# Performance work log

Measured on AMD Instinct MI355X. Metric: run time of the kernel, lower is better.

Reference implementation:

```python
import jax, jax.numpy as jnp
import numpy as np

N_NODES = 50000
N_EDGES = 800000
IN_DIM = 256
OUT_DIM = 64
HEADS = 4
NEG_SLOPE = 0.2  # PyG GATConv default


def setup_inputs() -> dict:
    key = jax.random.key(0)
    k_x, k_e, k_w, k_as, k_ad = jax.random.split(key, 5)
    x = jax.random.normal(k_x, (N_NODES, IN_DIM), dtype=jnp.float32)
    edge_index = jax.random.randint(k_e, (2, N_EDGES), 0, N_NODES, dtype=jnp.int64)
    # Glorot-ish scaled params (as in PyG GATConv)
    W = jax.random.normal(k_w, (IN_DIM, HEADS * OUT_DIM), dtype=jnp.float32) / np.sqrt(IN_DIM)
    att_src = jax.random.normal(k_as, (HEADS, OUT_DIM), dtype=jnp.float32) / np.sqrt(OUT_DIM)
    att_dst = jax.random.normal(k_ad, (HEADS, OUT_DIM), dtype=jnp.float32) / np.sqrt(OUT_DIM)
    bias = jnp.zeros((HEADS * OUT_DIM,), dtype=jnp.float32)
    return {"x": x, "edge_index": edge_index, "W": W,
            "att_src": att_src, "att_dst": att_dst, "bias": bias}


def reference(x, edge_index, W, att_src, att_dst, bias):
    N = x.shape[0]
    H, C = att_src.shape
    # add self-loops (PyG GATConv default add_self_loops=True)
    loop = jnp.arange(N, dtype=edge_index.dtype)
    src = jnp.concatenate([edge_index[0], loop])  # [E+N] message sources j
    dst = jnp.concatenate([edge_index[1], loop])  # [E+N] message targets i

    xh = (x @ W).reshape(N, H, C)                 # [N, H, C]
    a_src = jnp.einsum('nhc,hc->nh', xh, att_src)  # [N, H]
    a_dst = jnp.einsum('nhc,hc->nh', xh, att_dst)  # [N, H]

    logits = jax.nn.leaky_relu(a_src[src] + a_dst[dst], NEG_SLOPE)  # [E+N, H]
    # segment softmax over incoming edges of each destination node
    seg_max = jax.ops.segment_max(logits, dst, num_segments=N)      # [N, H]
    e = jnp.exp(logits - seg_max[dst])
    seg_sum = jax.ops.segment_sum(e, dst, num_segments=N)           # [N, H]
    alpha = e / seg_sum[dst]                                        # [E+N, H]

    # weighted scatter-aggregate of source features
    msgs = alpha[:, :, None] * xh[src]                              # [E+N, H, C]
    out = jax.ops.segment_sum(msgs, dst, num_segments=N)            # [N, H, C]
    out = out.reshape(N, H * C) + bias                              # concat heads + bias
    # h.dim() == 2 here, so the original's mean(dim=1) branch is not taken
    return out
```

## Files before the change

### kernel.cpp

```cpp
#include <hip/hip_runtime.h>

#define NEG_SLOPE 0.2f
#define LRELU(x) ((x) > 0.0f ? (x) : NEG_SLOPE * (x))

typedef short short8 __attribute__((ext_vector_type(8)));
typedef unsigned short ushort8 __attribute__((ext_vector_type(8)));
typedef float f32x4v __attribute__((ext_vector_type(4)));

__device__ __forceinline__ unsigned short f2bf(float f) {
  unsigned int u = __float_as_uint(f);
  unsigned int r = (u + 0x7FFFu + ((u >> 16) & 1u)) >> 16;
  return (unsigned short)r;
}

__device__ __forceinline__ float bf2f(unsigned short u) {
  return __uint_as_float(((unsigned int)u) << 16);
}

__device__ __forceinline__ unsigned int cvt_pk_bf16(float lo, float hi) {
  unsigned int r;
  asm("v_cvt_pk_bf16_f32 %0, %1, %2" : "=v"(r) : "v"(lo), "v"(hi));
  return r;
}

__device__ __forceinline__ void gload_lds16(const void* g, void* l) {
  __builtin_amdgcn_global_load_lds(
      (const __attribute__((address_space(1))) unsigned int*)g,
      (__attribute__((address_space(3))) unsigned int*)l, 16, 0, 0);
}

#define CBC 448
#define CBW 64
#define CBF 512

__global__ __launch_bounds__(256) void fused_pre(
    const float* __restrict__ W, unsigned short* __restrict__ Wtb,
    const int* __restrict__ ei, int* __restrict__ deg, int E) {
  int b = blockIdx.x;
  int tid = threadIdx.x;
  if (b < CBC) {
    for (int e = b * 256 + tid; e < E; e += CBC * 256)
      atomicAdd(&deg[ei[E + e]], 1);
  } else {
    int bb = b - CBC;
    for (int idx = bb * 256 + tid; idx < 256 * 256; idx += CBW * 256) {
      int n = idx >> 8, k = idx & 255;
      Wtb[n * 256 + k] = f2bf(W[k * 256 + n]);
    }
  }
}

__global__ __launch_bounds__(1024) void scan1_kernel(const int* __restrict__ deg,
                                                     int* __restrict__ row_start,
                                                     int* __restrict__ bsum, int N) {
  __shared__ int buf[1024];
  int i = blockIdx.x * 1024 + (int)threadIdx.x;
  int v = (i < N) ? deg[i] : 0;
  buf[threadIdx.x] = v;
  __syncthreads();
  int run = v;
  for (int off = 1; off < 1024; off <<= 1) {
    int t = ((int)threadIdx.x >= off) ? buf[threadIdx.x - off] : 0;
    __syncthreads();
    run += t;
    buf[threadIdx.x] = run;
    __syncthreads();
  }
  if (i < N) row_start[i] = run - v;
  if (threadIdx.x == 1023) bsum[blockIdx.x] = run;
}

__global__ __launch_bounds__(1024) void scan_off(int* __restrict__ row_start,
                                                 const int* __restrict__ bsum,
                                                 int nb, int N) {
  __shared__ int s_off;
  int b = blockIdx.x;
  if (threadIdx.x < 64) {
    int acc = 0;
    for (int j = (int)threadIdx.x; j < b; j += 64) acc += bsum[j];
    for (int off = 32; off; off >>= 1) acc += __shfl_down(acc, off, 64);
    if (threadIdx.x == 0) s_off = acc;
  }
  __syncthreads();
  int off = s_off;
  int i = b * 1024 + (int)threadIdx.x;
  if (i < N) row_start[i] += off;
  if (b == nb - 1 && threadIdx.x == 0) row_start[N] = off + bsum[b];
}

__global__ __launch_bounds__(256) void fused_main(
    const float* __restrict__ Xf, const unsigned short* __restrict__ Wtb,
    const float* __restrict__ attS, const float* __restrict__ attD,
    unsigned short* __restrict__ XHb, float* __restrict__ a_src,
    float* __restrict__ a_dst,
    const int* __restrict__ ei, const int* __restrict__ row_start,
    int* __restrict__ cursor, int* __restrict__ csr_src,
    int nGemm, int E, int N) {
  __shared__ unsigned short lA[128 * 32];
  __shared__ unsigned short lB[128 * 32];
  const int bid = blockIdx.x;
  const int tid = threadIdx.x;

  if (bid >= nGemm) {
    int bb = bid - nGemm;
    for (int e = bb * 256 + tid; e < E; e += CBF * 256) {
      int d = ei[E + e];
      int slot = row_start[d] + atomicAdd(&cursor[d], 1);
      csr_src[slot] = ei[e];
    }
    return;
  }

  const int lane = tid & 63;
  const int wave = tid >> 6;
  const int n0 = (bid & 1) * 128;
  const int m0 = (bid >> 1) * 128;
  const int wr = (wave >> 1) * 64;
  const int wc = (wave & 1) * 64;

  f32x4v acc[4][4];
#pragma unroll
  for (int i = 0; i < 4; ++i)
#pragma unroll
    for (int j = 0; j < 4; ++j) acc[i][j] = (f32x4v)(0.0f);

  const int srow = tid >> 2;
  const int skb = (tid & 3) * 16;
  const float* ap0 = Xf + (size_t)min(m0 + (tid >> 2), N - 1) * 256 + (tid & 3) * 8;
  const float* ap1 = Xf + (size_t)min(m0 + 64 + (tid >> 2), N - 1) * 256 + (tid & 3) * 8;

  const char* WtC = (const char*)Wtb;
  char* lAc = (char*)&lA[0];
  char* lBc = (char*)&lB[0];
  const int ldsB0 = wave * 1024;
  const int lr = lane & 15;
  const int hq = lane >> 4;
  const int kq = hq * 16;

  float4 c0 = *reinterpret_cast<const float4*>(ap0);
  float4 c1 = *reinterpret_cast<const float4*>(ap0 + 4);
  float4 c2 = *reinterpret_cast<const float4*>(ap1);
  float4 c3 = *reinterpret_cast<const float4*>(ap1 + 4);

#pragma unroll
  for (int kk = 0; kk < 8; ++kk) {
    const int k0 = kk * 32;
    gload_lds16(WtC + (size_t)(n0 + srow) * 512 + (size_t)k0 * 2 + skb, lBc + ldsB0);
    gload_lds16(WtC + (size_t)(n0 + srow + 64) * 512 + (size_t)k0 * 2 + skb,
                lBc + ldsB0 + 4096);
    {
      uint4 w0, w1;
      w0.x = cvt_pk_bf16(c0.x, c0.y); w0.y = cvt_pk_bf16(c0.z, c0.w);
      w0.z = cvt_pk_bf16(c1.x, c1.y); w0.w = cvt_pk_bf16(c1.z, c1.w);
      w1.x = cvt_pk_bf16(c2.x, c2.y); w1.y = cvt_pk_bf16(c2.z, c2.w);
      w1.z = cvt_pk_bf16(c3.x, c3.y); w1.w = cvt_pk_bf16(c3.z, c3.w);
      *reinterpret_cast<uint4*>(lAc + tid * 16) = w0;
      *reinterpret_cast<uint4*>(lAc + 4096 + tid * 16) = w1;
    }
    if (kk < 7) {
      c0 = *reinterpret_cast<const float4*>(ap0 + k0 + 32);
      c1 = *reinterpret_cast<const float4*>(ap0 + k0 + 36);
      c2 = *reinterpret_cast<const float4*>(ap1 + k0 + 32);
      c3 = *reinterpret_cast<const float4*>(ap1 + k0 + 36);
    }
    __syncthreads();

    short8 a[4], b[4];
#pragma unroll
    for (int i = 0; i < 4; ++i)
      a[i] = *reinterpret_cast<const short8*>(lAc + (wr + i * 16 + lr) * 64 + kq);
#pragma unroll
    for (int j = 0; j < 4; ++j)
      b[j] = *reinterpret_cast<const short8*>(lBc + (wc + j * 16 + lr) * 64 + kq);
#pragma unroll
    for (int i = 0; i < 4; ++i)
#pragma unroll
      for (int j = 0; j < 4; ++j)
        acc[i][j] = __builtin_amdgcn_mfma_f32_16x16x32_bf16(a[i], b[j], acc[i][j], 0, 0, 0);
    __syncthreads();
  }

  const int h = (n0 + wc) >> 6;
  float ws_[4], wd_[4];
#pragma unroll
  for (int j = 0; j < 4; ++j) {
    ws_[j] = attS[h * 64 + j * 16 + lr];
    wd_[j] = attD[h * 64 + j * 16 + lr];
  }
  const int rbase = m0 + wr + hq * 4;

#pragma unroll
  for (int i = 0; i < 4; ++i) {
#pragma unroll
    for (int r = 0; r < 4; ++r) {
      float ps = 0.f, pd = 0.f;
#pragma unroll
      for (int j = 0; j < 4; ++j) {
        ps += acc[i][j][r] * ws_[j];
        pd += acc[i][j][r] * wd_[j];
      }
#pragma unroll
      for (int off = 1; off < 16; off <<= 1) {
        ps += __shfl_xor(ps, off, 64);
        pd += __shfl_xor(pd, off, 64);
      }
      int row = rbase + i * 16 + r;
      if (lr == 0 && row < N) {
        a_src[row * 4 + h] = ps;
        a_dst[row * 4 + h] = pd;
      }
    }
  }

#pragma unroll
  for (int i = 0; i < 4; ++i)
#pragma unroll
    for (int j = 0; j < 4; ++j) {
      int col = n0 + wc + j * 16 + lr;
#pragma unroll
      for (int r = 0; r < 4; ++r)
        XHb[(size_t)(rbase + i * 16 + r) * 256 + col] = f2bf(acc[i][j][r]);
    }
}

__global__ __launch_bounds__(256) void gat_agg(
    const unsigned short* __restrict__ XHb, const float* __restrict__ a_src,
    const float* __restrict__ a_dst, const int* __restrict__ row_start,
    const int* __restrict__ csr_src, const float* __restrict__ bias,
    float* __restrict__ out, int N) {
  int wid = threadIdx.x >> 6;
  int lane = threadIdx.x & 63;
  int node = blockIdx.x * 4 + wid;
  if (node >= N) return;

  const int half = lane >> 5;
  const int l5 = lane & 31;
  const int h = l5 >> 3;
  const int c = l5 << 3;
  const unsigned short* __restrict__ xrow = XHb + c;

  float ad_h = a_dst[node * 4 + h];
  float as_h = a_src[node * 4 + h];

  int start = row_start[node];
  int end = row_start[node + 1];

  float acc[8];
  float sw = 0.f;
  if (half == 0) {
    float wself = __expf(LRELU(as_h + ad_h));
    ushort8 sv = *reinterpret_cast<const ushort8*>(xrow + (size_t)node * 256);
#pragma unroll
    for (int k = 0; k < 8; ++k) acc[k] = wself * bf2f(sv[k]);
    sw = wself;
  } else {
#pragma unroll
    for (int k = 0; k < 8; ++k) acc[k] = 0.f;
  }

  int p = start;
  for (; p + 8 <= end; p += 8) {
    int s0 = csr_src[p + half];
    int s1 = csr_src[p + 2 + half];
    int s2 = csr_src[p + 4 + half];
    int s3 = csr_src[p + 6 + half];
    float a0 = a_src[s0 * 4 + h] + ad_h;
    float a1 = a_src[s1 * 4 + h] + ad_h;
    float a2 = a_src[s2 * 4 + h] + ad_h;
    float a3 = a_src[s3 * 4 + h] + ad_h;
    ushort8 u0 = *reinterpret_cast<const ushort8*>(xrow + (size_t)s0 * 256);
    ushort8 u1 = *reinterpret_cast<const ushort8*>(xrow + (size_t)s1 * 256);
    ushort8 u2 = *reinterpret_cast<const ushort8*>(xrow + (size_t)s2 * 256);
    ushort8 u3 = *reinterpret_cast<const ushort8*>(xrow + (size_t)s3 * 256);
    float w0 = __expf(LRELU(a0));
    float w1 = __expf(LRELU(a1));
    float w2 = __expf(LRELU(a2));
    float w3 = __expf(LRELU(a3));
#pragma unroll
    for (int k = 0; k < 8; ++k) {
      acc[k] += w0 * bf2f(u0[k]);
      acc[k] += w1 * bf2f(u1[k]);
      acc[k] += w2 * bf2f(u2[k]);
      acc[k] += w3 * bf2f(u3[k]);
    }
    sw += (w0 + w1) + (w2 + w3);
  }
#pragma unroll
  for (int k = 0; k < 4; ++k) {
    int idx = p + 2 * k + half;
    if (idx < end) {
      int s = csr_src[idx];
      float aa = a_src[s * 4 + h] + ad_h;
      ushort8 u = *reinterpret_cast<const ushort8*>(xrow + (size_t)s * 256);
      float ww = __expf(LRELU(aa));
#pragma unroll
      for (int q = 0; q < 8; ++q) acc[q] += ww * bf2f(u[q]);
      sw += ww;
    }
  }

  sw += __shfl_xor(sw, 32, 64);
#pragma unroll
  for (int k = 0; k < 8; ++k) acc[k] += __shfl_xor(acc[k], 32, 64);

  if (half == 0) {
    float inv = 1.0f / sw;
    float4 b0 = *reinterpret_cast<const float4*>(bias + c);
    float4 b1 = *reinterpret_cast<const float4*>(bias + c + 4);
    float4 o0, o1;
    o0.x = acc[0] * inv + b0.x; o0.y = acc[1] * inv + b0.y;
    o0.z = acc[2] * inv + b0.z; o0.w = acc[3] * inv + b0.w;
    o1.x = acc[4] * inv + b1.x; o1.y = acc[5] * inv + b1.y;
    o1.z = acc[6] * inv + b1.z; o1.w = acc[7] * inv + b1.w;
    *reinterpret_cast<float4*>(out + (size_t)node * 256 + c) = o0;
    *reinterpret_cast<float4*>(out + (size_t)node * 256 + c + 4) = o1;
  }
}

extern "C" void kernel_launch(void* const* d_in, const int* in_sizes, int n_in,
                              void* d_out, int out_size, void* d_ws, size_t ws_size,
                              hipStream_t stream) {
  const float* x    = (const float*)d_in[0];
  const int*   ei   = (const int*)d_in[1];
  const float* Wm   = (const float*)d_in[2];
  const float* attS = (const float*)d_in[3];
  const float* attD = (const float*)d_in[4];
  const float* bias = (const float*)d_in[5];
  float* out = (float*)d_out;

  const int N = in_sizes[0] / 256;
  const int E = in_sizes[1] / 2;
  const int Mp = (N + 127) / 128 * 128;
  const int nb = (N + 1023) / 1024;

  char* w = (char*)d_ws;
  unsigned short* XHb = (unsigned short*)w;  w += (size_t)Mp * 256 * 2;
  unsigned short* Wtb = (unsigned short*)w;  w += (size_t)256 * 256 * 2;
  float* a_src = (float*)w;                  w += (size_t)N * 4 * 4;
  float* a_dst = (float*)w;                  w += (size_t)N * 4 * 4;
  int* deg = (int*)w;                        w += (size_t)N * 4;
  int* cursor = (int*)w;                     w += (size_t)N * 4;
  int* row_start = (int*)w;                  w += ((size_t)(N + 1) * 4 + 255) / 256 * 256;
  int* bsum = (int*)w;                       w += ((size_t)nb * 4 + 255) / 256 * 256;
  int* csr_src = (int*)w;                    w += (size_t)E * 4;

  hipMemsetAsync(deg, 0, (size_t)2 * N * 4, stream);

  fused_pre<<<CBC + CBW, 256, 0, stream>>>(Wm, Wtb, ei, deg, E);

  scan1_kernel<<<nb, 1024, 0, stream>>>(deg, row_start, bsum, N);
  scan_off<<<nb, 1024, 0, stream>>>(row_start, bsum, nb, N);

  const int nGemm = 2 * (Mp / 128);
  fused_main<<<nGemm + CBF, 256, 0, stream>>>(x, Wtb, attS, attD, XHb, a_src, a_dst,
                                              ei, row_start, cursor, csr_src,
                                              nGemm, E, N);

  gat_agg<<<(N + 3) / 4, 256, 0, stream>>>(XHb, a_src, a_dst, row_start, csr_src,
                                           bias, out, N);
}
```

Measured before the change: 174.5 us.

## Use a per-node insertion pointer for CSR fill, put scatter blocks first, and swizzle GEMM tiles

The scan now writes a copy of the row offsets into a 'next' array. The CSR fill can then take a slot with a single atomicAdd on next[d], so it no longer reads row_start and adds a separate cursor, and the memset of the cursor array is dropped. The scatter blocks move to the front of the grid and their count doubles. GEMM tiles are remapped so that groups of 8 M-tiles share each N-half, which should improve L2 reuse. M is padded to a multiple of 1024, so some extra padded GEMM tiles are launched.

```diff
diff --git a/kernel.cpp b/kernel.cpp
--- a/kernel.cpp
+++ b/kernel.cpp
@@ -31,7 +31,7 @@
 
 #define CBC 448
 #define CBW 64
-#define CBF 512
+#define CBF 1024
 
 __global__ __launch_bounds__(256) void fused_pre(
     const float* __restrict__ W, unsigned short* __restrict__ Wtb,
@@ -71,6 +71,7 @@
 }
 
 __global__ __launch_bounds__(1024) void scan_off(int* __restrict__ row_start,
+                                                 int* __restrict__ next,
                                                  const int* __restrict__ bsum,
                                                  int nb, int N) {
   __shared__ int s_off;
@@ -84,7 +85,11 @@
   __syncthreads();
   int off = s_off;
   int i = b * 1024 + (int)threadIdx.x;
-  if (i < N) row_start[i] += off;
+  if (i < N) {
+    int v = row_start[i] + off;
+    row_start[i] = v;
+    next[i] = v;
+  }
   if (b == nb - 1 && threadIdx.x == 0) row_start[N] = off + bsum[b];
 }
 
@@ -93,28 +98,27 @@
     const float* __restrict__ attS, const float* __restrict__ attD,
     unsigned short* __restrict__ XHb, float* __restrict__ a_src,
     float* __restrict__ a_dst,
-    const int* __restrict__ ei, const int* __restrict__ row_start,
-    int* __restrict__ cursor, int* __restrict__ csr_src,
-    int nGemm, int E, int N) {
+    const int* __restrict__ ei, int* __restrict__ next,
+    int* __restrict__ csr_src, int E, int N) {
   __shared__ unsigned short lA[128 * 32];
   __shared__ unsigned short lB[128 * 32];
   const int bid = blockIdx.x;
   const int tid = threadIdx.x;
 
-  if (bid >= nGemm) {
-    int bb = bid - nGemm;
-    for (int e = bb * 256 + tid; e < E; e += CBF * 256) {
+  if (bid < CBF) {
+    for (int e = bid * 256 + tid; e < E; e += CBF * 256) {
       int d = ei[E + e];
-      int slot = row_start[d] + atomicAdd(&cursor[d], 1);
+      int slot = atomicAdd(&next[d], 1);
       csr_src[slot] = ei[e];
     }
     return;
   }
 
+  const int gb = bid - CBF;
   const int lane = tid & 63;
   const int wave = tid >> 6;
-  const int n0 = (bid & 1) * 128;
-  const int m0 = (bid >> 1) * 128;
+  const int m0 = ((gb >> 4) * 8 + (gb & 7)) * 128;
+  const int n0 = ((gb >> 3) & 1) * 128;
   const int wr = (wave >> 1) * 64;
   const int wc = (wave & 1) * 64;
 
@@ -330,7 +334,7 @@
 
   const int N = in_sizes[0] / 256;
   const int E = in_sizes[1] / 2;
-  const int Mp = (N + 127) / 128 * 128;
+  const int Mp = (N + 1023) / 1024 * 1024;
   const int nb = (N + 1023) / 1024;
 
   char* w = (char*)d_ws;
@@ -339,22 +343,21 @@
   float* a_src = (float*)w;                  w += (size_t)N * 4 * 4;
   float* a_dst = (float*)w;                  w += (size_t)N * 4 * 4;
   int* deg = (int*)w;                        w += (size_t)N * 4;
-  int* cursor = (int*)w;                     w += (size_t)N * 4;
+  int* next = (int*)w;                       w += (size_t)N * 4;
   int* row_start = (int*)w;                  w += ((size_t)(N + 1) * 4 + 255) / 256 * 256;
   int* bsum = (int*)w;                       w += ((size_t)nb * 4 + 255) / 256 * 256;
   int* csr_src = (int*)w;                    w += (size_t)E * 4;
 
-  hipMemsetAsync(deg, 0, (size_t)2 * N * 4, stream);
+  hipMemsetAsync(deg, 0, (size_t)N * 4, stream);
 
   fused_pre<<<CBC + CBW, 256, 0, stream>>>(Wm, Wtb, ei, deg, E);
 
   scan1_kernel<<<nb, 1024, 0, stream>>>(deg, row_start, bsum, N);
-  scan_off<<<nb, 1024, 0, stream>>>(row_start, bsum, nb, N);
+  scan_off<<<nb, 1024, 0, stream>>>(row_start, next, bsum, nb, N);
 
   const int nGemm = 2 * (Mp / 128);
-  fused_main<<<nGemm + CBF, 256, 0, stream>>>(x, Wtb, attS, attD, XHb, a_src, a_dst,
-                                              ei, row_start, cursor, csr_src,
-                                              nGemm, E, N);
+  fused_main<<<CBF + nGemm, 256, 0, stream>>>(x, Wtb, attS, attD, XHb, a_src, a_dst,
+                                              ei, next, csr_src, E, N);
 
   gat_agg<<<(N + 3) / 4, 256, 0, stream>>>(XHb, a_src, a_dst, row_start, csr_src,
                                            bias, out, N);
```

After: 198.9 us. 1.14x slower.
